# Optimization experiments

Hardware: AMD Instinct MI355X
Metric: run time of the kernel (lower is better)

The kernel has to match this reference:

```python
import jax, jax.numpy as jnp
import numpy as np

B, L, H = 2, 2048, 1536
I, N, R, K = 3072, 16, 96, 4


def setup_inputs() -> dict:
    key = jax.random.key(0)
    ks = jax.random.split(key, 10)
    rn = lambda k, shape, s: jax.random.normal(k, shape, jnp.float32) * s
    return {
        "hidden_states": rn(ks[0], (B, L, H), 1.0),
        "W_in": rn(ks[1], (2 * I, H), 0.02),
        "conv_w": rn(ks[2], (I, K), 0.1),
        "conv_b": rn(ks[3], (I,), 0.1),
        "W_x": rn(ks[4], (R + 2 * N, I), 0.02),
        "W_dt": rn(ks[5], (I, R), 0.02),
        "dt_bias": rn(ks[6], (I,), 0.1),
        # vLLM's weight loader stores A = -exp(A_log); replicate that here
        "A": -jnp.exp(rn(ks[7], (I, N), 0.5)),
        "D": jnp.ones((I,), jnp.float32),
        "W_out": rn(ks[8], (H, I), 0.02),
    }


def reference(hidden_states, W_in, conv_w, conv_b, W_x, W_dt, dt_bias, A, D, W_out):
    b, l, _ = hidden_states.shape
    k = conv_w.shape[1]
    n = A.shape[1]
    r = W_dt.shape[1]

    # in_proj -> [B,L,2I], split into ssm input x and gate
    proj = jnp.einsum("blh,eh->ble", hidden_states, W_in)
    x, gate = jnp.split(proj, 2, axis=-1)  # each [B,L,I]

    # causal depthwise conv1d over L (pad K-1 on the left) + SiLU
    xp = jnp.pad(x, ((0, 0), (k - 1, 0), (0, 0)))
    conv = sum(xp[:, j : j + l, :] * conv_w[:, j] for j in range(k)) + conv_b
    x = jax.nn.silu(conv)  # [B,L,I]

    # x_proj -> dt (rank R), B, C (each N)
    ssm_p = jnp.einsum("bli,pi->blp", x, W_x)
    dt_in, Bm, Cm = jnp.split(ssm_p, [r, r + n], axis=-1)

    # dt_proj (skip_bias_add) then softplus(dt + bias) inside the scan math
    dt = jnp.einsum("blr,ir->bli", dt_in, W_dt)
    delta = jax.nn.softplus(dt + dt_bias)  # [B,L,I]

    # selective scan: s_t = exp(delta_t * A) * s_{t-1} + delta_t * x_t * B_t
    def step(state, inp):
        d_t, u_t, B_t, C_t = inp  # [B,I], [B,I], [B,N], [B,N]
        dA = jnp.exp(d_t[..., None] * A)  # [B,I,N]
        state = state * dA + (d_t * u_t)[..., None] * B_t[:, None, :]
        y = jnp.einsum("bin,bn->bi", state, C_t)
        return state, y

    init = jnp.zeros((b, x.shape[-1], n), jnp.float32)
    _, ys = jax.lax.scan(
        step,
        init,
        (
            delta.transpose(1, 0, 2),
            x.transpose(1, 0, 2),
            Bm.transpose(1, 0, 2),
            Cm.transpose(1, 0, 2),
        ),
    )
    y = ys.transpose(1, 0, 2) + x * D  # skip connection via D
    y = y * jax.nn.silu(gate)

    # out_proj -> [B,L,H]
    return jnp.einsum("bli,hi->blh", y, W_out)
```

## Files before the change

kernel.cpp:

```cpp
#include <hip/hip_runtime.h>

typedef __attribute__((ext_vector_type(8))) short bf16x8;
typedef __attribute__((ext_vector_type(4))) float f32x4;

#define CCH 32
#define TCH 64

__device__ __forceinline__ unsigned short f2b(float f) {
    unsigned u = __float_as_uint(f);
    return (unsigned short)((u + 0x7fffu + ((u >> 16) & 1u)) >> 16);
}
__device__ __forceinline__ float b2f(unsigned short h) {
    return __uint_as_float(((unsigned)h) << 16);
}
__device__ __forceinline__ float softplus_f(float z) {
    return (z > 15.f) ? z : __logf(1.f + __expf(z));
}
__device__ __forceinline__ float silu_f(float g) {
    return g / (1.f + __expf(-g));
}

__device__ __forceinline__ void gload16(const unsigned short* g, unsigned short* l) {
    __builtin_amdgcn_global_load_lds(
        (const __attribute__((address_space(1))) void*)g,
        (__attribute__((address_space(3))) void*)l, 16, 0, 0);
}

__global__ __launch_bounds__(256)
void cast_all(const float* __restrict__ h, const float* __restrict__ win,
              const float* __restrict__ wx, const float* __restrict__ wdt,
              const float* __restrict__ wout,
              unsigned short* __restrict__ dh, unsigned short* __restrict__ dwin,
              unsigned short* __restrict__ dwx, unsigned short* __restrict__ dwdt,
              unsigned short* __restrict__ dwout) {
    const int n0 = 1572864, n1 = n0 + 2359296, n2 = n1 + 98304,
              n3 = n2 + 73728, n4 = n3 + 1179648;
    int i = blockIdx.x * 256 + threadIdx.x;
    const float* s; unsigned short* d; int off;
    if (i < n0)      { s = h;    d = dh;    off = i; }
    else if (i < n1) { s = win;  d = dwin;  off = i - n0; }
    else if (i < n2) { s = wx;   d = dwx;   off = i - n1; }
    else if (i < n3) { s = wdt;  d = dwdt;  off = i - n2; }
    else if (i < n4) { s = wout; d = dwout; off = i - n3; }
    else return;
    float4 v = reinterpret_cast<const float4*>(s)[off];
    ushort4 o;
    o.x = f2b(v.x); o.y = f2b(v.y); o.z = f2b(v.z); o.w = f2b(v.w);
    reinterpret_cast<ushort4*>(d)[off] = o;
}

__global__ __launch_bounds__(512, 2)
void gemm_in(const unsigned short* __restrict__ A, const unsigned short* __restrict__ W,
             unsigned short* __restrict__ Cout, int Kc, int lda, int ldw, int ldc,
             int silu_col0) {
    __shared__ __align__(16) unsigned short A0s[8192];
    __shared__ __align__(16) unsigned short B0s[12288];
    __shared__ __align__(16) unsigned short A1s[8192];
    __shared__ __align__(16) unsigned short B1s[12288];
    const int tid  = threadIdx.x;
    const int lane = tid & 63;
    const int wave = tid >> 6;
    const int wr   = wave >> 2;
    const int wc   = wave & 3;
    const int lr   = lane & 15;
    const int quad = lane >> 4;
    const int sw2  = lr & 3;

    const int c  = blockIdx.x & 7;
    const int j  = blockIdx.x >> 3;
    const int bn = (c * 2 + (j & 1)) * 384;
    const int bm = (j >> 1) * 256;

    const int rsub = wave * 16 + (lane >> 2);
    const int csw  = ((lane & 3) ^ ((lane >> 2) & 3)) * 8;
    const unsigned short* gA = A + (size_t)(bm + rsub) * lda + csw;
    const unsigned short* gB = W + (size_t)(bn + rsub) * ldw + csw;

#define STAGE_A(ARR, kt) do { \
        gload16(gA + (size_t)0   * lda + (kt) * 32, ARR + wave * 512); \
        gload16(gA + (size_t)128 * lda + (kt) * 32, ARR + 4096 + wave * 512); \
    } while (0)
#define STAGE_B(ARR, kt) do { \
        gload16(gB + (size_t)0   * ldw + (kt) * 32, ARR + wave * 512); \
        gload16(gB + (size_t)128 * ldw + (kt) * 32, ARR + 4096 + wave * 512); \
        gload16(gB + (size_t)256 * ldw + (kt) * 32, ARR + 8192 + wave * 512); \
    } while (0)

#define LDA_F(ARR, mi) \
    (*reinterpret_cast<const bf16x8*>(&ARR[(wr * 128 + (mi) * 16 + lr) * 32 + ((quad ^ sw2)) * 8]))
#define LDB_F(ARR, ni) \
    (*reinterpret_cast<const bf16x8*>(&ARR[(wc * 96 + (ni) * 16 + lr) * 32 + ((quad ^ sw2)) * 8]))

#define PRIO1 __builtin_amdgcn_s_setprio(1)
#define PRIO0 __builtin_amdgcn_s_setprio(0)
#define VM0B  asm volatile("s_waitcnt vmcnt(0)\n\ts_barrier" ::: "memory")

#define TILE_BODY(AX, BX) do { \
        _Pragma("unroll") for (int ni = 0; ni < 6; ++ni) fb[ni] = LDB_F(BX, ni); \
        _Pragma("unroll") for (int mp = 0; mp < 4; ++mp) { \
            bf16x8 fa0 = LDA_F(AX, 2 * mp); \
            bf16x8 fa1 = LDA_F(AX, 2 * mp + 1); \
            PRIO1; \
            _Pragma("unroll") for (int ni = 0; ni < 6; ++ni) { \
                acc[2 * mp][ni]     = __builtin_amdgcn_mfma_f32_16x16x32_bf16(fa0, fb[ni], acc[2 * mp][ni], 0, 0, 0); \
                acc[2 * mp + 1][ni] = __builtin_amdgcn_mfma_f32_16x16x32_bf16(fa1, fb[ni], acc[2 * mp + 1][ni], 0, 0, 0); } \
            PRIO0; } \
    } while (0)

    f32x4 acc[8][6];
    const f32x4 zero = {0.f, 0.f, 0.f, 0.f};
#pragma unroll
    for (int m = 0; m < 8; ++m)
#pragma unroll
        for (int n = 0; n < 6; ++n) acc[m][n] = zero;

    bf16x8 fb[6];

    const int nkt = Kc >> 5;

    STAGE_A(A0s, 0); STAGE_B(B0s, 0);
    VM0B;

#pragma unroll 1
    for (int t = 0; t < nkt; t += 2) {
        if (t + 1 < nkt) { STAGE_A(A1s, t + 1); STAGE_B(B1s, t + 1); }
        TILE_BODY(A0s, B0s);
        VM0B;
        if (t + 1 < nkt) {
            if (t + 2 < nkt) { STAGE_A(A0s, t + 2); STAGE_B(B0s, t + 2); }
            TILE_BODY(A1s, B1s);
            VM0B;
        }
    }

#pragma unroll
    for (int mi = 0; mi < 8; ++mi) {
        const int row0 = bm + wr * 128 + mi * 16 + quad * 4;
#pragma unroll
        for (int ni = 0; ni < 6; ++ni) {
            const int col = bn + wc * 96 + ni * 16 + lr;
#pragma unroll
            for (int reg = 0; reg < 4; ++reg) {
                float v = acc[mi][ni][reg];
                if (col >= silu_col0) v = silu_f(v);
                Cout[(size_t)(row0 + reg) * ldc + col] = f2b(v);
            }
        }
    }
#undef STAGE_A
#undef STAGE_B
#undef LDA_F
#undef LDB_F
#undef PRIO1
#undef PRIO0
#undef VM0B
#undef TILE_BODY
}

__global__ __launch_bounds__(512)
void gemm_out(const unsigned short* __restrict__ A, const unsigned short* __restrict__ W,
              float* __restrict__ Cout, int Kc, int lda, int ldw, int ldc) {
    __shared__ __align__(16) unsigned short A0s[8192];
    __shared__ __align__(16) unsigned short B0s[12288];
    __shared__ __align__(16) unsigned short A1s[8192];
    __shared__ __align__(16) unsigned short B1s[12288];
    const int tid  = threadIdx.x;
    const int lane = tid & 63;
    const int wave = tid >> 6;
    const int wr   = wave >> 2;
    const int wc   = wave & 3;
    const int lr   = lane & 15;
    const int quad = lane >> 4;
    const int sw   = lr & 7;

    const int c  = blockIdx.x & 7;
    const int j  = blockIdx.x >> 3;
    const int bm = j * 128;
    const int bn = c * 192;

    const int rsub = wave * 8 + (lane >> 3);
    const int csw  = ((lane & 7) ^ ((lane >> 3) & 7)) * 8;
    const unsigned short* gA = A + (size_t)(bm + rsub) * lda + csw;
    const unsigned short* gB = W + (size_t)(bn + rsub) * ldw + csw;

#define STAGE_A(ARR, kt) do { \
        gload16(gA + (size_t)0  * lda + (kt) * 64, ARR + 0    + wave * 512); \
        gload16(gA + (size_t)64 * lda + (kt) * 64, ARR + 4096 + wave * 512); \
    } while (0)
#define STAGE_B(ARR, kt) do { \
        gload16(gB + (size_t)0   * ldw + (kt) * 64, ARR + 0    + wave * 512); \
        gload16(gB + (size_t)64  * ldw + (kt) * 64, ARR + 4096 + wave * 512); \
        gload16(gB + (size_t)128 * ldw + (kt) * 64, ARR + 8192 + wave * 512); \
    } while (0)

#define LDA_F(ARR, mi, kk) \
    (*reinterpret_cast<const bf16x8*>(&ARR[(wr * 64 + (mi) * 16 + lr) * 64 + (((((kk) << 2) | quad)) ^ sw) * 8]))
#define LDB_F(ARR, ni, kk) \
    (*reinterpret_cast<const bf16x8*>(&ARR[(wc * 48 + (ni) * 16 + lr) * 64 + (((((kk) << 2) | quad)) ^ sw) * 8]))

#define PRIO1 __builtin_amdgcn_s_setprio(1)
#define PRIO0 __builtin_amdgcn_s_setprio(0)
#define VM0B  asm volatile("s_waitcnt vmcnt(0)\n\ts_barrier" ::: "memory")

#define TILE_BODY(AX, BX) do { \
        _Pragma("unroll") for (int ni = 0; ni < 3; ++ni) { \
            fb[ni][0] = LDB_F(BX, ni, 0); fb[ni][1] = LDB_F(BX, ni, 1); } \
        _Pragma("unroll") for (int mi = 0; mi < 4; ++mi) { \
            fa[mi][0] = LDA_F(AX, mi, 0); fa[mi][1] = LDA_F(AX, mi, 1); } \
        PRIO1; \
        _Pragma("unroll") for (int mi = 0; mi < 4; ++mi) \
        _Pragma("unroll") for (int ni = 0; ni < 3; ++ni) { \
            acc[mi][ni] = __builtin_amdgcn_mfma_f32_16x16x32_bf16(fa[mi][0], fb[ni][0], acc[mi][ni], 0, 0, 0); \
            acc[mi][ni] = __builtin_amdgcn_mfma_f32_16x16x32_bf16(fa[mi][1], fb[ni][1], acc[mi][ni], 0, 0, 0); } \
        PRIO0; \
    } while (0)

    f32x4 acc[4][3];
    const f32x4 zero = {0.f, 0.f, 0.f, 0.f};
#pragma unroll
    for (int m = 0; m < 4; ++m)
#pragma unroll
        for (int n = 0; n < 3; ++n) acc[m][n] = zero;

    bf16x8 fa[4][2], fb[3][2];

    const int nkt = Kc >> 6;

    STAGE_A(A0s, 0); STAGE_B(B0s, 0);
    VM0B;

#pragma unroll 1
    for (int t = 0; t < nkt; t += 2) {
        if (t + 1 < nkt) { STAGE_A(A1s, t + 1); STAGE_B(B1s, t + 1); }
        TILE_BODY(A0s, B0s);
        VM0B;
        if (t + 1 < nkt) {
            if (t + 2 < nkt) { STAGE_A(A0s, t + 2); STAGE_B(B0s, t + 2); }
            TILE_BODY(A1s, B1s);
            VM0B;
        }
    }

#pragma unroll
    for (int mi = 0; mi < 4; ++mi) {
        const int row0 = bm + wr * 64 + mi * 16 + quad * 4;
#pragma unroll
        for (int ni = 0; ni < 3; ++ni) {
            const int col = bn + wc * 48 + ni * 16 + lr;
#pragma unroll
            for (int reg = 0; reg < 4; ++reg)
                Cout[(size_t)(row0 + reg) * ldc + col] = acc[mi][ni][reg];
        }
    }
#undef STAGE_A
#undef STAGE_B
#undef LDA_F
#undef LDB_F
#undef PRIO1
#undef PRIO0
#undef VM0B
#undef TILE_BODY
}

template <int OP>
__global__ __launch_bounds__(256)
void gemm_mfma(const unsigned short* __restrict__ A, const unsigned short* __restrict__ W,
               void* __restrict__ Cout, int Kc, int lda, int ldw, int ldc,
               const float* __restrict__ bias, int silu_col0, long long czs) {
    __shared__ unsigned short As[3][4096];
    __shared__ unsigned short Bs[3][4096];
    const int tid = threadIdx.x;
    const int bm = blockIdx.y * 128;
    const int bn = blockIdx.x * 128;
    const int kz = blockIdx.z;
    A += (size_t)kz * Kc;
    W += (size_t)kz * Kc;
    const int lane = tid & 63;
    const int wave = tid >> 6;
    const int r_a = lane >> 2;
    const int k8 = (lane & 3) * 8;

    const unsigned short* gA0 = A + (size_t)(bm + wave * 16 + r_a) * lda + k8;
    const unsigned short* gA1 = A + (size_t)(bm + 64 + wave * 16 + r_a) * lda + k8;
    const unsigned short* gB0 = W + (size_t)(bn + wave * 16 + r_a) * ldw + k8;
    const unsigned short* gB1 = W + (size_t)(bn + 64 + wave * 16 + r_a) * ldw + k8;

    const int wm = (wave & 1) * 64;
    const int wn = (wave >> 1) * 64;
    const int lr = lane & 15;
    const int quad = lane >> 4;

    f32x4 acc[4][4];
    const f32x4 zero = {0.f, 0.f, 0.f, 0.f};
#pragma unroll
    for (int i = 0; i < 4; i++)
#pragma unroll
        for (int j = 0; j < 4; j++) acc[i][j] = zero;

#define STAGE(koff, j) do { \
        gload16(gA0 + (koff), As[j] + wave * 512); \
        gload16(gA1 + (koff), As[j] + (wave + 4) * 512); \
        gload16(gB0 + (koff), Bs[j] + wave * 512); \
        gload16(gB1 + (koff), Bs[j] + (wave + 4) * 512); \
    } while (0)

    const int niter = Kc >> 5;
    STAGE(0, 0);
    if (niter > 1) STAGE(32, 1);

    int ib = 0;
    for (int k = 0; k < niter; k++) {
        if (k + 1 < niter)
            asm volatile("s_waitcnt vmcnt(4)\n\ts_barrier" ::: "memory");
        else
            asm volatile("s_waitcnt vmcnt(0)\n\ts_barrier" ::: "memory");
        if (k + 2 < niter) {
            int is_ = ib + 2; if (is_ >= 3) is_ -= 3;
            STAGE((k + 2) << 5, is_);
        }
        const unsigned short* as = As[ib];
        const unsigned short* bs = Bs[ib];
        bf16x8 fa[4], fb[4];
#pragma unroll
        for (int mi = 0; mi < 4; mi++)
            fa[mi] = *reinterpret_cast<const bf16x8*>(as + (wm + mi * 16 + lr) * 32 + quad * 8);
#pragma unroll
        for (int ni = 0; ni < 4; ni++)
            fb[ni] = *reinterpret_cast<const bf16x8*>(bs + (wn + ni * 16 + lr) * 32 + quad * 8);
#pragma unroll
        for (int mi = 0; mi < 4; mi++)
#pragma unroll
            for (int ni = 0; ni < 4; ni++)
                acc[mi][ni] = __builtin_amdgcn_mfma_f32_16x16x32_bf16(fa[mi], fb[ni], acc[mi][ni], 0, 0, 0);
        ib = (ib == 2) ? 0 : ib + 1;
    }
#undef STAGE

#pragma unroll
    for (int mi = 0; mi < 4; mi++)
#pragma unroll
        for (int reg = 0; reg < 4; reg++) {
            int row = bm + wm + mi * 16 + quad * 4 + reg;
#pragma unroll
            for (int ni = 0; ni < 4; ni++) {
                int col = bn + wn + ni * 16 + lr;
                float v = acc[mi][ni][reg];
                if (OP == 0) {
                    float* Cf = (float*)Cout + (size_t)kz * czs;
                    Cf[(size_t)row * ldc + col] = v;
                } else if (OP == 2) {
                    if (col >= silu_col0) v = silu_f(v);
                    ((unsigned short*)Cout)[(size_t)row * ldc + col] = f2b(v);
                } else {
                    ((unsigned short*)Cout)[(size_t)row * ldc + col] = f2b(softplus_f(v + bias[col]));
                }
            }
        }
}

__global__ __launch_bounds__(256)
void reduce_xpart(const float* __restrict__ xpart, float* __restrict__ ssmp,
                  unsigned short* __restrict__ dtin) {
    const int BL = 4096;
    int idx = blockIdx.x * 256 + threadIdx.x;
    int row = idx >> 5;
    int c4 = (idx & 31) * 4;
    float4 s = {0.f, 0.f, 0.f, 0.f};
#pragma unroll
    for (int z = 0; z < 8; z++) {
        float4 v = *reinterpret_cast<const float4*>(xpart + (size_t)z * BL * 128 + (size_t)row * 128 + c4);
        s.x += v.x; s.y += v.y; s.z += v.z; s.w += v.w;
    }
    *reinterpret_cast<float4*>(ssmp + (size_t)row * 128 + c4) = s;
    if (c4 < 96) {
        ushort4 o;
        o.x = f2b(s.x); o.y = f2b(s.y); o.z = f2b(s.z); o.w = f2b(s.w);
        *reinterpret_cast<ushort4*>(dtin + (size_t)row * 96 + c4) = o;
    }
}

__global__ __launch_bounds__(256)
void conv_silu8(const unsigned short* __restrict__ projbf, const float* __restrict__ cw,
                const float* __restrict__ cb, unsigned short* __restrict__ xc) {
    const int I = 3072, L = 2048, LD = 6144;
    int idx = blockIdx.x * 256 + threadIdx.x;
    int i8 = (idx % (I / 8)) * 8;
    int bl = idx / (I / 8);
    int l = bl & (L - 1);
    float s[8];
    {
        float4 b0 = *reinterpret_cast<const float4*>(cb + i8);
        float4 b1 = *reinterpret_cast<const float4*>(cb + i8 + 4);
        s[0]=b0.x; s[1]=b0.y; s[2]=b0.z; s[3]=b0.w; s[4]=b1.x; s[5]=b1.y; s[6]=b1.z; s[7]=b1.w;
    }
    float w[8][4];
#pragma unroll
    for (int c = 0; c < 8; c++) {
        float4 wr = *reinterpret_cast<const float4*>(cw + (i8 + c) * 4);
        w[c][0]=wr.x; w[c][1]=wr.y; w[c][2]=wr.z; w[c][3]=wr.w;
    }
#pragma unroll
    for (int j = 0; j < 4; j++) {
        if (l + j - 3 >= 0) {
            uint4 r = *reinterpret_cast<const uint4*>(projbf + (size_t)(bl + j - 3) * LD + i8);
            float xv[8];
            xv[0]=b2f((unsigned short)(r.x & 0xffff)); xv[1]=b2f((unsigned short)(r.x >> 16));
            xv[2]=b2f((unsigned short)(r.y & 0xffff)); xv[3]=b2f((unsigned short)(r.y >> 16));
            xv[4]=b2f((unsigned short)(r.z & 0xffff)); xv[5]=b2f((unsigned short)(r.z >> 16));
            xv[6]=b2f((unsigned short)(r.w & 0xffff)); xv[7]=b2f((unsigned short)(r.w >> 16));
#pragma unroll
            for (int c = 0; c < 8; c++) s[c] = fmaf(xv[c], w[c][j], s[c]);
        }
    }
    unsigned short o[8];
#pragma unroll
    for (int c = 0; c < 8; c++) o[c] = f2b(silu_f(s[c]));
    uint4 packed;
    packed.x = (unsigned)o[0] | ((unsigned)o[1] << 16);
    packed.y = (unsigned)o[2] | ((unsigned)o[3] << 16);
    packed.z = (unsigned)o[4] | ((unsigned)o[5] << 16);
    packed.w = (unsigned)o[6] | ((unsigned)o[7] << 16);
    *reinterpret_cast<uint4*>(xc + (size_t)bl * I + i8) = packed;
}

__global__ __launch_bounds__(256)
void scan_passA(const unsigned short* __restrict__ delta_bf, const unsigned short* __restrict__ xc,
                const float* __restrict__ ssmp, const float* __restrict__ Aw,
                float* __restrict__ S_local, float* __restrict__ sumDelta) {
    const int I = 3072, L = 2048, HI = 1536;
    __shared__ float bc[TCH][16];
    int g = blockIdx.x * 256 + threadIdx.x;
    int i = g % HI;
    int bcid = g / HI;
    int c = bcid % CCH;
    int b = bcid / CCH;
    size_t rowbase = (size_t)b * L + (size_t)c * TCH;
    {
        int e = threadIdx.x;
        int t = e >> 2, q = e & 3;
        float4 v = *reinterpret_cast<const float4*>(ssmp + (rowbase + t) * 128 + 96 + q * 4);
        *reinterpret_cast<float4*>(&bc[t][q * 4]) = v;
    }
    __syncthreads();

    float A0[16], A1[16], s0[16], s1[16];
#pragma unroll
    for (int n = 0; n < 16; n++) {
        A0[n] = Aw[i * 16 + n];
        A1[n] = Aw[(i + HI) * 16 + n];
        s0[n] = 0.f; s1[n] = 0.f;
    }
    float sum0 = 0.f, sum1 = 0.f;

    size_t rowI = rowbase * I + i;
    for (int t = 0; t < TCH; t++) {
        float d0 = b2f(delta_bf[rowI]);
        float d1 = b2f(delta_bf[rowI + HI]);
        float du0 = d0 * b2f(xc[rowI]);
        float du1 = d1 * b2f(xc[rowI + HI]);
        sum0 += d0; sum1 += d1;
        float4 b0 = *reinterpret_cast<const float4*>(&bc[t][0]);
        float4 b1v = *reinterpret_cast<const float4*>(&bc[t][4]);
        float4 b2 = *reinterpret_cast<const float4*>(&bc[t][8]);
        float4 b3 = *reinterpret_cast<const float4*>(&bc[t][12]);
        const float bv[16] = {b0.x,b0.y,b0.z,b0.w, b1v.x,b1v.y,b1v.z,b1v.w,
                              b2.x,b2.y,b2.z,b2.w, b3.x,b3.y,b3.z,b3.w};
#pragma unroll
        for (int n = 0; n < 16; n++) {
            s0[n] = fmaf(s0[n], __expf(d0 * A0[n]), du0 * bv[n]);
            s1[n] = fmaf(s1[n], __expf(d1 * A1[n]), du1 * bv[n]);
        }
        rowI += I;
    }
    size_t obase = (size_t)bcid * 16 * I + i;
#pragma unroll
    for (int n = 0; n < 16; n++) {
        S_local[obase + (size_t)n * I]      = s0[n];
        S_local[obase + (size_t)n * I + HI] = s1[n];
    }
    sumDelta[(size_t)bcid * I + i]      = sum0;
    sumDelta[(size_t)bcid * I + i + HI] = sum1;
}

__global__ __launch_bounds__(256)
void scan_passB(const float* __restrict__ S_local, const float* __restrict__ sumDelta,
                const float* __restrict__ Aw, float* __restrict__ state_in) {
    const int I = 3072;
    int g = blockIdx.x * 256 + threadIdx.x;
    int i = g % I;
    int bn = g / I;
    int n = bn & 15;
    int b = bn >> 4;
    float a = Aw[i * 16 + n];
    float state = 0.f;
    for (int c = 0; c < CCH; c++) {
        int bcid = b * CCH + c;
        size_t idx = ((size_t)bcid * 16 + n) * I + i;
        state_in[idx] = state;
        state = fmaf(state, __expf(a * sumDelta[(size_t)bcid * I + i]), S_local[idx]);
    }
}

__global__ __launch_bounds__(256)
void scan_passC(const unsigned short* __restrict__ projbf,
                const unsigned short* __restrict__ xc,
                const float* __restrict__ ssmp, const unsigned short* __restrict__ delta_bf,
                const float* __restrict__ Aw, const float* __restrict__ Dw,
                const float* __restrict__ state_in, unsigned short* __restrict__ ybf) {
    const int I = 3072, L = 2048, LD = 6144, HI = 1536;
    __shared__ float bc[TCH][32];
    int g = blockIdx.x * 256 + threadIdx.x;
    int i = g % HI;
    int bcid = g / HI;
    int c = bcid % CCH;
    int b = bcid / CCH;
    size_t rowbase = (size_t)b * L + (size_t)c * TCH;
    for (int e = threadIdx.x; e < TCH * 8; e += 256) {
        int t = e >> 3, q = e & 7;
        float4 v = *reinterpret_cast<const float4*>(ssmp + (rowbase + t) * 128 + 96 + q * 4);
        *reinterpret_cast<float4*>(&bc[t][q * 4]) = v;
    }
    __syncthreads();

    float A0[16], A1[16], s0[16], s1[16];
#pragma unroll
    for (int n = 0; n < 16; n++) {
        A0[n] = Aw[i * 16 + n];
        A1[n] = Aw[(i + HI) * 16 + n];
    }
    float D0 = Dw[i], D1 = Dw[i + HI];
    size_t sbase = (size_t)bcid * 16 * I + i;
#pragma unroll
    for (int n = 0; n < 16; n++) {
        s0[n] = state_in[sbase + (size_t)n * I];
        s1[n] = state_in[sbase + (size_t)n * I + HI];
    }

    size_t rowI = rowbase * I + i;
    size_t rowG = rowbase * LD + I + i;
    for (int t = 0; t < TCH; t++) {
        float d0 = b2f(delta_bf[rowI]);
        float d1 = b2f(delta_bf[rowI + HI]);
        float u0 = b2f(xc[rowI]);
        float u1 = b2f(xc[rowI + HI]);
        float du0 = d0 * u0, du1 = d1 * u1;
        float4 v0 = *reinterpret_cast<const float4*>(&bc[t][0]);
        float4 v1 = *reinterpret_cast<const float4*>(&bc[t][4]);
        float4 v2 = *reinterpret_cast<const float4*>(&bc[t][8]);
        float4 v3 = *reinterpret_cast<const float4*>(&bc[t][12]);
        float4 w0 = *reinterpret_cast<const float4*>(&bc[t][16]);
        float4 w1 = *reinterpret_cast<const float4*>(&bc[t][20]);
        float4 w2 = *reinterpret_cast<const float4*>(&bc[t][24]);
        float4 w3 = *reinterpret_cast<const float4*>(&bc[t][28]);
        const float bv[16] = {v0.x,v0.y,v0.z,v0.w, v1.x,v1.y,v1.z,v1.w,
                              v2.x,v2.y,v2.z,v2.w, v3.x,v3.y,v3.z,v3.w};
        const float cv[16] = {w0.x,w0.y,w0.z,w0.w, w1.x,w1.y,w1.z,w1.w,
                              w2.x,w2.y,w2.z,w2.w, w3.x,w3.y,w3.z,w3.w};
        float y0 = 0.f, y1 = 0.f;
#pragma unroll
        for (int n = 0; n < 16; n++) {
            s0[n] = fmaf(s0[n], __expf(d0 * A0[n]), du0 * bv[n]);
            s1[n] = fmaf(s1[n], __expf(d1 * A1[n]), du1 * bv[n]);
            y0 = fmaf(s0[n], cv[n], y0);
            y1 = fmaf(s1[n], cv[n], y1);
        }
        y0 = fmaf(u0, D0, y0);
        y1 = fmaf(u1, D1, y1);
        y0 *= b2f(projbf[rowG]);
        y1 *= b2f(projbf[rowG + HI]);
        ybf[rowI]      = f2b(y0);
        ybf[rowI + HI] = f2b(y1);
        rowI += I;
        rowG += LD;
    }
}

extern "C" void kernel_launch(void* const* d_in, const int* in_sizes, int n_in,
                              void* d_out, int out_size, void* d_ws, size_t ws_size,
                              hipStream_t stream) {
    const float* hidden  = (const float*)d_in[0];
    const float* W_in    = (const float*)d_in[1];
    const float* conv_w  = (const float*)d_in[2];
    const float* conv_b  = (const float*)d_in[3];
    const float* W_x     = (const float*)d_in[4];
    const float* W_dt    = (const float*)d_in[5];
    const float* dt_bias = (const float*)d_in[6];
    const float* Aw      = (const float*)d_in[7];
    const float* Dw      = (const float*)d_in[8];
    const float* W_out   = (const float*)d_in[9];
    float* out = (float*)d_out;

    constexpr int Bsz = 2, L = 2048, H = 1536, I = 3072, R = 96;
    constexpr int BL = Bsz * L;
    constexpr int TwoI = 2 * I;

    char* base = (char*)d_ws;
    unsigned short* proj_bf  = (unsigned short*)base; base += (size_t)BL * TwoI * 2;
    unsigned short* delta_bf = (unsigned short*)base; base += (size_t)BL * I * 2;
    unsigned short* xc_bf    = (unsigned short*)base; base += (size_t)BL * I * 2;
    unsigned short* y_bf     = (unsigned short*)base; base += (size_t)BL * I * 2;
    float* ssmp              = (float*)base;          base += (size_t)BL * 128 * 4;
    float* xpart             = (float*)base;          base += (size_t)8 * BL * 128 * 4;
    unsigned short* dtin_bf  = (unsigned short*)base; base += (size_t)BL * R * 2;
    unsigned short* wx_bf    = (unsigned short*)base; base += (size_t)128 * I * 2;
    unsigned short* wdt_bf   = (unsigned short*)base; base += (size_t)I * R * 2;
    unsigned short* wout_bf  = (unsigned short*)base; base += (size_t)H * I * 2;
    unsigned short* h_bf     = (unsigned short*)base; base += (size_t)BL * H * 2;
    unsigned short* win_bf   = (unsigned short*)base; base += (size_t)TwoI * H * 2;
    float* S_local  = (float*)h_bf;
    float* sumDelta = S_local + (size_t)Bsz * CCH * 16 * I;
    float* state_in = sumDelta + (size_t)Bsz * CCH * I;

    dim3 blk(256);

    cast_all<<<(5283840 + 255) / 256, blk, 0, stream>>>(
        hidden, W_in, W_x, W_dt, W_out, h_bf, win_bf, wx_bf, wdt_bf, wout_bf);

    gemm_in<<<dim3(256, 1, 1), dim3(512), 0, stream>>>(
        h_bf, win_bf, proj_bf, H, H, H, TwoI,  I);

    conv_silu8<<<BL * I / 8 / 256, blk, 0, stream>>>(proj_bf, conv_w, conv_b, xc_bf);

    gemm_mfma<0><<<dim3(1, BL / 128, 8), blk, 0, stream>>>(
        xc_bf, wx_bf, xpart, I / 8, I, I, 128, nullptr, 0, (long long)BL * 128);
    reduce_xpart<<<BL * 32 / 256, blk, 0, stream>>>(xpart, ssmp, dtin_bf);

    gemm_mfma<3><<<dim3(I / 128, BL / 128, 1), blk, 0, stream>>>(
        dtin_bf, wdt_bf, delta_bf, R, R, R, I, dt_bias, 0, 0);

    scan_passA<<<Bsz * CCH * (I / 2) / 256, blk, 0, stream>>>(
        delta_bf, xc_bf, ssmp, Aw, S_local, sumDelta);
    scan_passB<<<Bsz * 16 * I / 256, blk, 0, stream>>>(
        S_local, sumDelta, Aw, state_in);
    scan_passC<<<Bsz * CCH * (I / 2) / 256, blk, 0, stream>>>(
        proj_bf, xc_bf, ssmp, delta_bf, Aw, Dw, state_in, y_bf);

    gemm_out<<<dim3(256, 1, 1), dim3(512), 0, stream>>>(
        y_bf, wout_bf, out, I, I, I, H);
}
```

Baseline: 478.7 us.

## Use one channel per thread in scan passes and retune gemm_in LDS swizzle

The scan passA and passC kernels drop the two-channels-per-thread layout and give each thread a single channel, which doubles the thread count and halves per-thread registers and state. The aim is higher occupancy and more parallelism to hide the latency of the serial time loop. Separately, the gemm_in LDS XOR swizzle now derives its key from different lane bits, to change the bank-conflict pattern of its fragment reads. The cost is less per-thread instruction-level parallelism in the scan and more duplicated shared-memory B/C reads.

New measurement: 451.9 us. -5.6%, faster.

```diff
diff --git a/kernel.cpp b/kernel.cpp
--- a/kernel.cpp
+++ b/kernel.cpp
@@ -64,7 +64,7 @@
     const int wc   = wave & 3;
     const int lr   = lane & 15;
     const int quad = lane >> 4;
-    const int sw2  = lr & 3;
+    const int sw2  = (lr >> 1) & 3;
 
     const int c  = blockIdx.x & 7;
     const int j  = blockIdx.x >> 3;
@@ -72,7 +72,7 @@
     const int bm = (j >> 1) * 256;
 
     const int rsub = wave * 16 + (lane >> 2);
-    const int csw  = ((lane & 3) ^ ((lane >> 2) & 3)) * 8;
+    const int csw  = ((lane & 3) ^ ((lane >> 3) & 3)) * 8;
     const unsigned short* gA = A + (size_t)(bm + rsub) * lda + csw;
     const unsigned short* gB = W + (size_t)(bn + rsub) * ldw + csw;
 
@@ -427,59 +427,49 @@
 void scan_passA(const unsigned short* __restrict__ delta_bf, const unsigned short* __restrict__ xc,
                 const float* __restrict__ ssmp, const float* __restrict__ Aw,
                 float* __restrict__ S_local, float* __restrict__ sumDelta) {
-    const int I = 3072, L = 2048, HI = 1536;
-    __shared__ float bc[TCH][16];
+    const int I = 3072, L = 2048;
+    __shared__ float bc[TCH][32];
     int g = blockIdx.x * 256 + threadIdx.x;
-    int i = g % HI;
-    int bcid = g / HI;
+    int i = g % I;
+    int bcid = g / I;
     int c = bcid % CCH;
     int b = bcid / CCH;
     size_t rowbase = (size_t)b * L + (size_t)c * TCH;
-    {
-        int e = threadIdx.x;
-        int t = e >> 2, q = e & 3;
+    for (int e = threadIdx.x; e < TCH * 8; e += 256) {
+        int t = e >> 3, q = e & 7;
         float4 v = *reinterpret_cast<const float4*>(ssmp + (rowbase + t) * 128 + 96 + q * 4);
         *reinterpret_cast<float4*>(&bc[t][q * 4]) = v;
     }
     __syncthreads();
 
-    float A0[16], A1[16], s0[16], s1[16];
-#pragma unroll
-    for (int n = 0; n < 16; n++) {
-        A0[n] = Aw[i * 16 + n];
-        A1[n] = Aw[(i + HI) * 16 + n];
-        s0[n] = 0.f; s1[n] = 0.f;
-    }
-    float sum0 = 0.f, sum1 = 0.f;
+    float Arow[16];
+#pragma unroll
+    for (int n = 0; n < 16; n++) Arow[n] = Aw[i * 16 + n];
+    float st[16];
+#pragma unroll
+    for (int n = 0; n < 16; n++) st[n] = 0.f;
+    float sumD = 0.f;
 
     size_t rowI = rowbase * I + i;
     for (int t = 0; t < TCH; t++) {
-        float d0 = b2f(delta_bf[rowI]);
-        float d1 = b2f(delta_bf[rowI + HI]);
-        float du0 = d0 * b2f(xc[rowI]);
-        float du1 = d1 * b2f(xc[rowI + HI]);
-        sum0 += d0; sum1 += d1;
+        float delta = b2f(delta_bf[rowI]);
+        float du = delta * b2f(xc[rowI]);
+        sumD += delta;
         float4 b0 = *reinterpret_cast<const float4*>(&bc[t][0]);
-        float4 b1v = *reinterpret_cast<const float4*>(&bc[t][4]);
+        float4 b1 = *reinterpret_cast<const float4*>(&bc[t][4]);
         float4 b2 = *reinterpret_cast<const float4*>(&bc[t][8]);
         float4 b3 = *reinterpret_cast<const float4*>(&bc[t][12]);
-        const float bv[16] = {b0.x,b0.y,b0.z,b0.w, b1v.x,b1v.y,b1v.z,b1v.w,
+        const float bv[16] = {b0.x,b0.y,b0.z,b0.w, b1.x,b1.y,b1.z,b1.w,
                               b2.x,b2.y,b2.z,b2.w, b3.x,b3.y,b3.z,b3.w};
 #pragma unroll
-        for (int n = 0; n < 16; n++) {
-            s0[n] = fmaf(s0[n], __expf(d0 * A0[n]), du0 * bv[n]);
-            s1[n] = fmaf(s1[n], __expf(d1 * A1[n]), du1 * bv[n]);
-        }
+        for (int n = 0; n < 16; n++)
+            st[n] = fmaf(st[n], __expf(delta * Arow[n]), du * bv[n]);
         rowI += I;
     }
     size_t obase = (size_t)bcid * 16 * I + i;
 #pragma unroll
-    for (int n = 0; n < 16; n++) {
-        S_local[obase + (size_t)n * I]      = s0[n];
-        S_local[obase + (size_t)n * I + HI] = s1[n];
-    }
-    sumDelta[(size_t)bcid * I + i]      = sum0;
-    sumDelta[(size_t)bcid * I + i + HI] = sum1;
+    for (int n = 0; n < 16; n++) S_local[obase + (size_t)n * I] = st[n];
+    sumDelta[(size_t)bcid * I + i] = sumD;
 }
 
 __global__ __launch_bounds__(256)
@@ -507,11 +497,11 @@
                 const float* __restrict__ ssmp, const unsigned short* __restrict__ delta_bf,
                 const float* __restrict__ Aw, const float* __restrict__ Dw,
                 const float* __restrict__ state_in, unsigned short* __restrict__ ybf) {
-    const int I = 3072, L = 2048, LD = 6144, HI = 1536;
+    const int I = 3072, L = 2048, LD = 6144;
     __shared__ float bc[TCH][32];
     int g = blockIdx.x * 256 + threadIdx.x;
-    int i = g % HI;
-    int bcid = g / HI;
+    int i = g % I;
+    int bcid = g / I;
     int c = bcid % CCH;
     int b = bcid / CCH;
     size_t rowbase = (size_t)b * L + (size_t)c * TCH;
@@ -522,54 +512,42 @@
     }
     __syncthreads();
 
-    float A0[16], A1[16], s0[16], s1[16];
-#pragma unroll
-    for (int n = 0; n < 16; n++) {
-        A0[n] = Aw[i * 16 + n];
-        A1[n] = Aw[(i + HI) * 16 + n];
-    }
-    float D0 = Dw[i], D1 = Dw[i + HI];
+    float Arow[16];
+#pragma unroll
+    for (int n = 0; n < 16; n++) Arow[n] = Aw[i * 16 + n];
+    float Dv = Dw[i];
+    float st[16];
     size_t sbase = (size_t)bcid * 16 * I + i;
 #pragma unroll
-    for (int n = 0; n < 16; n++) {
-        s0[n] = state_in[sbase + (size_t)n * I];
-        s1[n] = state_in[sbase + (size_t)n * I + HI];
-    }
+    for (int n = 0; n < 16; n++) st[n] = state_in[sbase + (size_t)n * I];
 
     size_t rowI = rowbase * I + i;
     size_t rowG = rowbase * LD + I + i;
     for (int t = 0; t < TCH; t++) {
-        float d0 = b2f(delta_bf[rowI]);
-        float d1 = b2f(delta_bf[rowI + HI]);
-        float u0 = b2f(xc[rowI]);
-        float u1 = b2f(xc[rowI + HI]);
-        float du0 = d0 * u0, du1 = d1 * u1;
-        float4 v0 = *reinterpret_cast<const float4*>(&bc[t][0]);
-        float4 v1 = *reinterpret_cast<const float4*>(&bc[t][4]);
-        float4 v2 = *reinterpret_cast<const float4*>(&bc[t][8]);
-        float4 v3 = *reinterpret_cast<const float4*>(&bc[t][12]);
-        float4 w0 = *reinterpret_cast<const float4*>(&bc[t][16]);
-        float4 w1 = *reinterpret_cast<const float4*>(&bc[t][20]);
-        float4 w2 = *reinterpret_cast<const float4*>(&bc[t][24]);
-        float4 w3 = *reinterpret_cast<const float4*>(&bc[t][28]);
-        const float bv[16] = {v0.x,v0.y,v0.z,v0.w, v1.x,v1.y,v1.z,v1.w,
-                              v2.x,v2.y,v2.z,v2.w, v3.x,v3.y,v3.z,v3.w};
-        const float cv[16] = {w0.x,w0.y,w0.z,w0.w, w1.x,w1.y,w1.z,w1.w,
-                              w2.x,w2.y,w2.z,w2.w, w3.x,w3.y,w3.z,w3.w};
-        float y0 = 0.f, y1 = 0.f;
+        float delta = b2f(delta_bf[rowI]);
+        float u = b2f(xc[rowI]);
+        float du = delta * u;
+        float4 b0 = *reinterpret_cast<const float4*>(&bc[t][0]);
+        float4 b1 = *reinterpret_cast<const float4*>(&bc[t][4]);
+        float4 b2 = *reinterpret_cast<const float4*>(&bc[t][8]);
+        float4 b3 = *reinterpret_cast<const float4*>(&bc[t][12]);
+        float4 c0 = *reinterpret_cast<const float4*>(&bc[t][16]);
+        float4 c1 = *reinterpret_cast<const float4*>(&bc[t][20]);
+        float4 c2 = *reinterpret_cast<const float4*>(&bc[t][24]);
+        float4 c3 = *reinterpret_cast<const float4*>(&bc[t][28]);
+        const float bv[16] = {b0.x,b0.y,b0.z,b0.w, b1.x,b1.y,b1.z,b1.w,
+                              b2.x,b2.y,b2.z,b2.w, b3.x,b3.y,b3.z,b3.w};
+        const float cv[16] = {c0.x,c0.y,c0.z,c0.w, c1.x,c1.y,c1.z,c1.w,
+                              c2.x,c2.y,c2.z,c2.w, c3.x,c3.y,c3.z,c3.w};
+        float y = 0.f;
 #pragma unroll
         for (int n = 0; n < 16; n++) {
-            s0[n] = fmaf(s0[n], __expf(d0 * A0[n]), du0 * bv[n]);
-            s1[n] = fmaf(s1[n], __expf(d1 * A1[n]), du1 * bv[n]);
-            y0 = fmaf(s0[n], cv[n], y0);
-            y1 = fmaf(s1[n], cv[n], y1);
-        }
-        y0 = fmaf(u0, D0, y0);
-        y1 = fmaf(u1, D1, y1);
-        y0 *= b2f(projbf[rowG]);
-        y1 *= b2f(projbf[rowG + HI]);
-        ybf[rowI]      = f2b(y0);
-        ybf[rowI + HI] = f2b(y1);
+            st[n] = fmaf(st[n], __expf(delta * Arow[n]), du * bv[n]);
+            y = fmaf(st[n], cv[n], y);
+        }
+        y = fmaf(u, Dv, y);
+        y *= b2f(projbf[rowG]);
+        ybf[rowI] = f2b(y);
         rowI += I;
         rowG += LD;
     }
@@ -628,11 +606,11 @@
     gemm_mfma<3><<<dim3(I / 128, BL / 128, 1), blk, 0, stream>>>(
         dtin_bf, wdt_bf, delta_bf, R, R, R, I, dt_bias, 0, 0);
 
-    scan_passA<<<Bsz * CCH * (I / 2) / 256, blk, 0, stream>>>(
+    scan_passA<<<Bsz * I * CCH / 256, blk, 0, stream>>>(
         delta_bf, xc_bf, ssmp, Aw, S_local, sumDelta);
     scan_passB<<<Bsz * 16 * I / 256, blk, 0, stream>>>(
         S_local, sumDelta, Aw, state_in);
-    scan_passC<<<Bsz * CCH * (I / 2) / 256, blk, 0, stream>>>(
+    scan_passC<<<Bsz * I * CCH / 256, blk, 0, stream>>>(
         proj_bf, xc_bf, ssmp, delta_bf, Aw, Dw, state_in, y_bf);
 
     gemm_out<<<dim3(256, 1, 1), dim3(512), 0, stream>>>(
```
